# Kernel optimization log

Hardware: AMD Instinct MI355X
Metric: run time of the kernel (lower is better)

## Reference

```python
import jax, jax.numpy as jnp
import numpy as np

N_USERS = 100000
N_ITEMS = 50000
DIM = 64
N_EDGES = 1000000
N_NODES = N_USERS + N_ITEMS


def setup_inputs() -> dict:
    key = jax.random.key(0)
    k1, k2, k3 = jax.random.split(key, 3)
    # nn.init.normal_(std=0.1)
    user_emb = jax.random.normal(k1, (N_USERS, DIM), dtype=jnp.float32) * 0.1
    item_emb = jax.random.normal(k2, (N_ITEMS, DIM), dtype=jnp.float32) * 0.1
    edge_index = jax.random.randint(k3, (2, N_EDGES), 0, N_NODES, dtype=jnp.int32)
    return {"user_emb": user_emb, "item_emb": item_emb,
            "edge_index": edge_index, "n_layers": 3}


def reference(user_emb, item_emb, edge_index, n_layers):
    """LightGCN.computer(): n_layers of LGConv with uniform-alpha residual sum."""
    num_users = user_emb.shape[0]
    x = jnp.concatenate([user_emb, item_emb], axis=0)  # [N, d]
    n = x.shape[0]
    src, dst = edge_index[0], edge_index[1]

    # gcn_norm without self-loops (PyG LGConv default): deg from dst (in-degree)
    deg = jax.ops.segment_sum(jnp.ones_like(dst, dtype=x.dtype), dst,
                              num_segments=n)  # [N]
    dinv = jnp.where(deg > 0, jax.lax.rsqrt(jnp.maximum(deg, 1.0)), 0.0)
    norm = dinv[src] * dinv[dst]  # [E]

    alpha = 1.0 / (n_layers + 1)
    out = x * alpha
    for _ in range(n_layers):
        msg = x[src] * norm[:, None]                          # gather + scale [E, d]
        x = jax.ops.segment_sum(msg, dst, num_segments=n)     # scatter-add  [N, d]
        out = out + x * alpha
    users = out[:num_users]
    items = out[num_users:]
    return users, items
```

## Files before the change

### kernel.cpp

```cpp
#include <hip/hip_runtime.h>


#define N_USERS_C 100000
#define NNODES_C  150000
#define DIM_C     64
#define NLAYERS_C 3

#define BSHIFT    10
#define BSIZE     1024
#define NB_BUCKET ((NNODES_C + BSIZE - 1) >> BSHIFT)
#define EPB       4096
#define NBLK_E    ((1000000 + EPB - 1) / EPB)
#define HIST_N    (NB_BUCKET * NBLK_E)
#define SCAN_L1B  ((HIST_N + 1023) / 1024)


__device__ __forceinline__ float bf2f(unsigned short u) {
    union { unsigned int i; float f; } c;
    c.i = ((unsigned int)u) << 16;
    return c.f;
}

__device__ __forceinline__ unsigned short f2bf(float f) {
    union { float f; unsigned int i; } c;
    c.f = f;
    unsigned int x = c.i;
    return (unsigned short)((x + 0x7fffu + ((x >> 16) & 1u)) >> 16);
}


__global__ void k_hist(const int* __restrict__ dst, int* __restrict__ hist, int nE) {
    __shared__ int sh[NB_BUCKET];
    for (int i = threadIdx.x; i < NB_BUCKET; i += 256) sh[i] = 0;
    __syncthreads();
    int gEnd = min((int)(blockIdx.x + 1) * (EPB / 4), nE / 4);
    for (int g = blockIdx.x * (EPB / 4) + threadIdx.x; g < gEnd; g += 256) {
        int4 d4 = *(const int4*)(dst + g * 4);
        atomicAdd(&sh[d4.x >> BSHIFT], 1);
        atomicAdd(&sh[d4.y >> BSHIFT], 1);
        atomicAdd(&sh[d4.z >> BSHIFT], 1);
        atomicAdd(&sh[d4.w >> BSHIFT], 1);
    }
    __syncthreads();
    for (int b = threadIdx.x; b < NB_BUCKET; b += 256)
        hist[b * NBLK_E + blockIdx.x] = sh[b];
}

__global__ void k_scan_l1(int* __restrict__ hist, int* __restrict__ l1sum) {
    __shared__ int sd[1024];
    int t = threadIdx.x;
    int i = blockIdx.x * 1024 + t;
    int v = (i < HIST_N) ? hist[i] : 0;
    sd[t] = v;
    __syncthreads();
    for (int o = 1; o < 1024; o <<= 1) {
        int u = (t >= o) ? sd[t - o] : 0;
        __syncthreads();
        sd[t] += u;
        __syncthreads();
    }
    if (i < HIST_N) hist[i] = sd[t] - v;
    if (t == 1023) l1sum[blockIdx.x] = sd[1023];
}

__global__ void k_scan_l2add(int* __restrict__ hist, const int* __restrict__ l1sum) {
    __shared__ int s_pre;
    int t = threadIdx.x;
    if (t < 64) {
        int v = (t < (int)blockIdx.x && t < SCAN_L1B) ? l1sum[t] : 0;
        #pragma unroll
        for (int m = 1; m < 64; m <<= 1) v += __shfl_xor(v, m);
        if (t == 0) s_pre = v;
    }
    __syncthreads();
    int i = blockIdx.x * 1024 + t;
    if (i < HIST_N) hist[i] += s_pre;
}

__global__ void k_bucket(const int* __restrict__ src, const int* __restrict__ dst,
                         const int* __restrict__ histS, unsigned int* __restrict__ staged,
                         int nE) {
    __shared__ int sc[NB_BUCKET];
    for (int b = threadIdx.x; b < NB_BUCKET; b += 256)
        sc[b] = histS[b * NBLK_E + blockIdx.x];
    __syncthreads();
    int gEnd = min((int)(blockIdx.x + 1) * (EPB / 4), nE / 4);
    for (int g = blockIdx.x * (EPB / 4) + threadIdx.x; g < gEnd; g += 256) {
        int4 s4 = *(const int4*)(src + g * 4);
        int4 d4 = *(const int4*)(dst + g * 4);
        int p;
        p = atomicAdd(&sc[d4.x >> BSHIFT], 1);
        staged[p] = ((unsigned int)s4.x << BSHIFT) | (unsigned int)(d4.x & (BSIZE - 1));
        p = atomicAdd(&sc[d4.y >> BSHIFT], 1);
        staged[p] = ((unsigned int)s4.y << BSHIFT) | (unsigned int)(d4.y & (BSIZE - 1));
        p = atomicAdd(&sc[d4.z >> BSHIFT], 1);
        staged[p] = ((unsigned int)s4.z << BSHIFT) | (unsigned int)(d4.z & (BSIZE - 1));
        p = atomicAdd(&sc[d4.w >> BSHIFT], 1);
        staged[p] = ((unsigned int)s4.w << BSHIFT) | (unsigned int)(d4.w & (BSIZE - 1));
    }
}

__global__ void k_csr(const int* __restrict__ histS, const unsigned int* __restrict__ staged,
                      int* __restrict__ off, int* __restrict__ csrS,
                      int nE, int nNodes) {
    __shared__ int s_deg[BSIZE];
    __shared__ int s_scan[BSIZE];
    int b = blockIdx.x;
    int t = threadIdx.x;
    int base = histS[b * NBLK_E];
    int end  = (b + 1 < NB_BUCKET) ? histS[(b + 1) * NBLK_E] : nE;
    int cnt  = end - base;

    s_deg[t] = 0;
    __syncthreads();
    for (int k = t; k < cnt; k += BSIZE) {
        unsigned int w = staged[base + k];
        atomicAdd(&s_deg[w & (BSIZE - 1)], 1);
    }
    __syncthreads();
    int v = s_deg[t];
    s_scan[t] = v;
    __syncthreads();
    for (int o = 1; o < BSIZE; o <<= 1) {
        int u = (t >= o) ? s_scan[t - o] : 0;
        __syncthreads();
        s_scan[t] += u;
        __syncthreads();
    }
    int ex = s_scan[t] - v;
    int node = (b << BSHIFT) + t;
    if (node < nNodes) off[node] = base + ex;
    if (b == 0 && t == 0) off[nNodes] = nE;
    s_deg[t] = ex;
    __syncthreads();
    for (int k = t; k < cnt; k += BSIZE) {
        unsigned int w = staged[base + k];
        int slot = base + atomicAdd(&s_deg[w & (BSIZE - 1)], 1);
        csrS[slot] = (int)(w >> BSHIFT);
    }
}


__global__ void k_cvt(const float4* __restrict__ ue, const float4* __restrict__ ie,
                      const int* __restrict__ off, uint4* __restrict__ t0,
                      int n8u, int n8) {
    int i = blockIdx.x * blockDim.x + threadIdx.x;
    if (i >= n8) return;
    int node = i >> 3;
    int dg = off[node + 1] - off[node];
    float dv = (dg > 0) ? rsqrtf((float)dg) : 0.0f;
    float4 a, b;
    if (i < n8u) { a = ue[2 * i];         b = ue[2 * i + 1]; }
    else         { a = ie[2 * (i - n8u)]; b = ie[2 * (i - n8u) + 1]; }
    uint4 o;
    o.x = (unsigned int)f2bf(a.x * dv) | ((unsigned int)f2bf(a.y * dv) << 16);
    o.y = (unsigned int)f2bf(a.z * dv) | ((unsigned int)f2bf(a.w * dv) << 16);
    o.z = (unsigned int)f2bf(b.x * dv) | ((unsigned int)f2bf(b.y * dv) << 16);
    o.w = (unsigned int)f2bf(b.z * dv) | ((unsigned int)f2bf(b.w * dv) << 16);
    t0[i] = o;
}


__device__ __forceinline__ void add8(float* a, uint4 v) {
    a[0] += bf2f((unsigned short)(v.x & 0xffff));
    a[1] += bf2f((unsigned short)(v.x >> 16));
    a[2] += bf2f((unsigned short)(v.y & 0xffff));
    a[3] += bf2f((unsigned short)(v.y >> 16));
    a[4] += bf2f((unsigned short)(v.z & 0xffff));
    a[5] += bf2f((unsigned short)(v.z >> 16));
    a[6] += bf2f((unsigned short)(v.w & 0xffff));
    a[7] += bf2f((unsigned short)(v.w >> 16));
}

__device__ __forceinline__ void fma8(float* a, uint4 v, float w) {
    a[0] += w * bf2f((unsigned short)(v.x & 0xffff));
    a[1] += w * bf2f((unsigned short)(v.x >> 16));
    a[2] += w * bf2f((unsigned short)(v.y & 0xffff));
    a[3] += w * bf2f((unsigned short)(v.y >> 16));
    a[4] += w * bf2f((unsigned short)(v.z & 0xffff));
    a[5] += w * bf2f((unsigned short)(v.z >> 16));
    a[6] += w * bf2f((unsigned short)(v.w & 0xffff));
    a[7] += w * bf2f((unsigned short)(v.w >> 16));
}

template <int FINAL>
__global__ void k_gather(const int* __restrict__ off, const int* __restrict__ csrS,
                         const unsigned short* __restrict__ T,
                         unsigned short* __restrict__ Tn,
                         const float* __restrict__ ue, const float* __restrict__ ie,
                         const unsigned short* __restrict__ T0,
                         const unsigned short* __restrict__ T1,
                         float* __restrict__ outp, float alpha, int nNodes) {
    int t = blockIdx.x * blockDim.x + threadIdx.x;
    int w = t >> 6;
    int lane = t & 63;
    int half = lane >> 5;
    int sub  = lane & 31;
    int slot = sub >> 3;
    int q    = sub & 7;
    int node = w * 2 + half;
    if (node >= nNodes) return;

    int b = off[node];
    int e = off[node + 1];

    float a[8] = {0.f, 0.f, 0.f, 0.f, 0.f, 0.f, 0.f, 0.f};

    for (int jj = b; jj < e; jj += 4) {
        int j = jj + slot;
        if (j < e) {
            int s = csrS[j];
            uint4 v = *(const uint4*)(T + (size_t)s * DIM_C + q * 8);
            add8(a, v);
        }
    }

    #pragma unroll
    for (int m = 8; m <= 16; m <<= 1) {
        #pragma unroll
        for (int k = 0; k < 8; ++k) a[k] += __shfl_xor(a[k], m);
    }

    if (slot == 0) {
        size_t idx = (size_t)node * DIM_C + q * 8;
        float degf = (float)(e - b);
        if (FINAL) {
            float r[8] = {0.f, 0.f, 0.f, 0.f, 0.f, 0.f, 0.f, 0.f};
            float dv = 0.0f;
            if (e > b) {
                float sd = sqrtf(degf);
                dv = rsqrtf(degf);
                uint4 u0 = *(const uint4*)(T0 + idx);
                uint4 u1 = *(const uint4*)(T1 + idx);
                uint4 u2 = *(const uint4*)(T + idx);
                fma8(r, u0, sd);
                fma8(r, u1, sd);
                fma8(r, u2, sd);
            } else {
                const float* ob = (node < N_USERS_C)
                    ? (ue + (size_t)node * DIM_C + q * 8)
                    : (ie + (size_t)(node - N_USERS_C) * DIM_C + q * 8);
                float4 x0a = *(const float4*)(ob);
                float4 x0b = *(const float4*)(ob + 4);
                r[0] = x0a.x; r[1] = x0a.y; r[2] = x0a.z; r[3] = x0a.w;
                r[4] = x0b.x; r[5] = x0b.y; r[6] = x0b.z; r[7] = x0b.w;
            }
            float4 o0, o1;
            o0.x = alpha * (r[0] + dv * a[0]);
            o0.y = alpha * (r[1] + dv * a[1]);
            o0.z = alpha * (r[2] + dv * a[2]);
            o0.w = alpha * (r[3] + dv * a[3]);
            o1.x = alpha * (r[4] + dv * a[4]);
            o1.y = alpha * (r[5] + dv * a[5]);
            o1.z = alpha * (r[6] + dv * a[6]);
            o1.w = alpha * (r[7] + dv * a[7]);
            *(float4*)(outp + idx)     = o0;
            *(float4*)(outp + idx + 4) = o1;
        } else {
            float inv = (e > b) ? (1.0f / degf) : 0.0f;
            uint4 o;
            o.x = (unsigned int)f2bf(a[0] * inv) | ((unsigned int)f2bf(a[1] * inv) << 16);
            o.y = (unsigned int)f2bf(a[2] * inv) | ((unsigned int)f2bf(a[3] * inv) << 16);
            o.z = (unsigned int)f2bf(a[4] * inv) | ((unsigned int)f2bf(a[5] * inv) << 16);
            o.w = (unsigned int)f2bf(a[6] * inv) | ((unsigned int)f2bf(a[7] * inv) << 16);
            *(uint4*)(Tn + idx) = o;
        }
    }
}


__global__ void k_count_deg_fb(const int* __restrict__ dst, int* __restrict__ deg, int nE) {
    int e = blockIdx.x * blockDim.x + threadIdx.x;
    if (e < nE) atomicAdd(&deg[dst[e]], 1);
}

__global__ void k_dinv_fb(const int* __restrict__ deg, float* __restrict__ dinv, int n) {
    int i = blockIdx.x * blockDim.x + threadIdx.x;
    if (i < n) {
        int d = deg[i];
        dinv[i] = (d > 0) ? rsqrtf((float)d) : 0.0f;
    }
}

__global__ void k_init_fb(const float4* __restrict__ ue, const float4* __restrict__ ie,
                          float4* __restrict__ x, float4* __restrict__ out,
                          float alpha, int n4u, int n4) {
    int i = blockIdx.x * blockDim.x + threadIdx.x;
    if (i < n4) {
        float4 v = (i < n4u) ? ue[i] : ie[i - n4u];
        x[i] = v;
        out[i] = make_float4(v.x * alpha, v.y * alpha, v.z * alpha, v.w * alpha);
    }
}

__global__ void k_scatter(const int* __restrict__ src, const int* __restrict__ dst,
                          const float* __restrict__ dinv, const float* __restrict__ x,
                          float* __restrict__ y, int nE) {
    int t = blockIdx.x * blockDim.x + threadIdx.x;
    int e = t >> 4;
    int q = t & 15;
    if (e >= nE) return;
    int s = src[e];
    int d = dst[e];
    float w = dinv[s] * dinv[d];
    float4 v = *(const float4*)(x + (size_t)s * DIM_C + q * 4);
    float* yp = y + (size_t)d * DIM_C + q * 4;
    atomicAdd(yp + 0, v.x * w);
    atomicAdd(yp + 1, v.y * w);
    atomicAdd(yp + 2, v.z * w);
    atomicAdd(yp + 3, v.w * w);
}

__global__ void k_accum(const float4* __restrict__ y, float4* __restrict__ out,
                        float alpha, int n4) {
    int i = blockIdx.x * blockDim.x + threadIdx.x;
    if (i < n4) {
        float4 v = y[i];
        float4 o = out[i];
        o.x += v.x * alpha;
        o.y += v.y * alpha;
        o.z += v.z * alpha;
        o.w += v.w * alpha;
        out[i] = o;
    }
}


extern "C" void kernel_launch(void* const* d_in, const int* in_sizes, int n_in,
                              void* d_out, int out_size, void* d_ws, size_t ws_size,
                              hipStream_t stream) {
    const float* user_emb = (const float*)d_in[0];
    const float* item_emb = (const float*)d_in[1];
    const int*   edge     = (const int*)d_in[2];

    const int nE = in_sizes[2] / 2;
    const int* src = edge;
    const int* dst = edge + nE;

    const int nNodes = NNODES_C;
    const int nElems = nNodes * DIM_C;
    const int n4     = nElems / 4;
    const int n4u    = N_USERS_C * DIM_C / 4;
    const float alpha = 1.0f / (NLAYERS_C + 1);
    float* out = (float*)d_out;

    const size_t REQ = 66344448;

    char* ws = (char*)d_ws;

    if (ws_size >= REQ) {
        int*            hist   = (int*)           (ws);
        int*            l1sum  = (int*)           (ws + 144064);
        unsigned int*   staged = (unsigned int*)  (ws + 144320);
        int*            off    = (int*)           (ws + 4144320);
        int*            csrS   = (int*)           (ws + 4744336);
        unsigned short* T0     = (unsigned short*)(ws + 8744448);
        unsigned short* T1     = (unsigned short*)(ws + 27944448);
        unsigned short* T2     = (unsigned short*)(ws + 47144448);

        k_hist<<<NBLK_E, 256, 0, stream>>>(dst, hist, nE);
        k_scan_l1<<<SCAN_L1B, 1024, 0, stream>>>(hist, l1sum);
        k_scan_l2add<<<SCAN_L1B, 1024, 0, stream>>>(hist, l1sum);
        k_bucket<<<NBLK_E, 256, 0, stream>>>(src, dst, hist, staged, nE);
        k_csr<<<NB_BUCKET, BSIZE, 0, stream>>>(hist, staged, off, csrS, nE, nNodes);

        const int n8  = nElems / 8;
        const int n8u = N_USERS_C * DIM_C / 8;
        k_cvt<<<(n8 + 255) / 256, 256, 0, stream>>>(
            (const float4*)user_emb, (const float4*)item_emb, off, (uint4*)T0, n8u, n8);

        const int gwaves  = (nNodes + 1) / 2;
        const int gblocks = (gwaves * 64 + 255) / 256;
        k_gather<0><<<gblocks, 256, 0, stream>>>(off, csrS, T0, T1,
                                                 nullptr, nullptr, nullptr, nullptr,
                                                 nullptr, alpha, nNodes);
        k_gather<0><<<gblocks, 256, 0, stream>>>(off, csrS, T1, T2,
                                                 nullptr, nullptr, nullptr, nullptr,
                                                 nullptr, alpha, nNodes);
        k_gather<1><<<gblocks, 256, 0, stream>>>(off, csrS, T2, nullptr,
                                                 user_emb, item_emb, T0, T1,
                                                 out, alpha, nNodes);
    } else {
        int*   deg  = (int*)  (ws);
        float* dinv = (float*)(ws + 600000);
        float* xbuf = (float*)(ws + 1200000);
        float* ybuf = (float*)(ws + 1200000 + (size_t)nElems * 4);

        hipMemsetAsync(deg, 0, (size_t)nNodes * sizeof(int), stream);
        k_count_deg_fb<<<(nE + 255) / 256, 256, 0, stream>>>(dst, deg, nE);
        k_dinv_fb<<<(nNodes + 255) / 256, 256, 0, stream>>>(deg, dinv, nNodes);
        k_init_fb<<<(n4 + 255) / 256, 256, 0, stream>>>(
            (const float4*)user_emb, (const float4*)item_emb,
            (float4*)xbuf, (float4*)out, alpha, n4u, n4);

        float* xb = xbuf;
        float* yb = ybuf;
        const int scatterThreads = nE * 16;
        for (int l = 0; l < NLAYERS_C; ++l) {
            hipMemsetAsync(yb, 0, (size_t)nElems * sizeof(float), stream);
            k_scatter<<<(scatterThreads + 255) / 256, 256, 0, stream>>>(
                src, dst, dinv, xb, yb, nE);
            k_accum<<<(n4 + 255) / 256, 256, 0, stream>>>(
                (const float4*)yb, (float4*)out, alpha, n4);
            float* tmp = xb; xb = yb; yb = tmp;
        }
    }
}
```

Before: 147.8 us.

## Fuse histogram, scan and bucketing into one kernel using fixed-capacity buckets

Replaces the separate histogram, two-level scan and bucket-scatter kernels with a single kernel. Each block counts locally, then reserves space in fixed-capacity per-bucket regions through global atomics. k_csr now computes the global bucket prefix from the bucket counts. This drops several kernel launches and a pass over dst, at the cost of a memset, more workspace, and a hard cap of 16384 edges per bucket that could overflow on skewed inputs.

```diff
diff --git a/kernel.cpp b/kernel.cpp
--- a/kernel.cpp
+++ b/kernel.cpp
@@ -9,10 +9,10 @@
 #define BSHIFT    10
 #define BSIZE     1024
 #define NB_BUCKET ((NNODES_C + BSIZE - 1) >> BSHIFT)
+#define CAPSHIFT  14
+#define CAP       (1 << CAPSHIFT)
 #define EPB       4096
 #define NBLK_E    ((1000000 + EPB - 1) / EPB)
-#define HIST_N    (NB_BUCKET * NBLK_E)
-#define SCAN_L1B  ((HIST_N + 1023) / 1024)
 
 
 __device__ __forceinline__ float bf2f(unsigned short u) {
@@ -29,97 +29,69 @@
 }
 
 
-__global__ void k_hist(const int* __restrict__ dst, int* __restrict__ hist, int nE) {
-    __shared__ int sh[NB_BUCKET];
-    for (int i = threadIdx.x; i < NB_BUCKET; i += 256) sh[i] = 0;
-    __syncthreads();
-    int gEnd = min((int)(blockIdx.x + 1) * (EPB / 4), nE / 4);
-    for (int g = blockIdx.x * (EPB / 4) + threadIdx.x; g < gEnd; g += 256) {
+__global__ void k_bucket2(const int* __restrict__ src, const int* __restrict__ dst,
+                          int* __restrict__ bcnt, unsigned int* __restrict__ staged,
+                          int nE) {
+    __shared__ int s_cnt[NB_BUCKET];
+    __shared__ int s_cur[NB_BUCKET];
+    int t = threadIdx.x;
+    for (int i = t; i < NB_BUCKET; i += 256) s_cnt[i] = 0;
+    __syncthreads();
+
+    int nE4  = nE >> 2;
+    int g0   = blockIdx.x * (EPB / 4) + t;
+    int gEnd = min((int)(blockIdx.x + 1) * (EPB / 4), nE4);
+
+    for (int g = g0; g < gEnd; g += 256) {
         int4 d4 = *(const int4*)(dst + g * 4);
-        atomicAdd(&sh[d4.x >> BSHIFT], 1);
-        atomicAdd(&sh[d4.y >> BSHIFT], 1);
-        atomicAdd(&sh[d4.z >> BSHIFT], 1);
-        atomicAdd(&sh[d4.w >> BSHIFT], 1);
-    }
-    __syncthreads();
-    for (int b = threadIdx.x; b < NB_BUCKET; b += 256)
-        hist[b * NBLK_E + blockIdx.x] = sh[b];
-}
-
-__global__ void k_scan_l1(int* __restrict__ hist, int* __restrict__ l1sum) {
-    __shared__ int sd[1024];
-    int t = threadIdx.x;
-    int i = blockIdx.x * 1024 + t;
-    int v = (i < HIST_N) ? hist[i] : 0;
-    sd[t] = v;
-    __syncthreads();
-    for (int o = 1; o < 1024; o <<= 1) {
-        int u = (t >= o) ? sd[t - o] : 0;
-        __syncthreads();
-        sd[t] += u;
-        __syncthreads();
-    }
-    if (i < HIST_N) hist[i] = sd[t] - v;
-    if (t == 1023) l1sum[blockIdx.x] = sd[1023];
-}
-
-__global__ void k_scan_l2add(int* __restrict__ hist, const int* __restrict__ l1sum) {
-    __shared__ int s_pre;
-    int t = threadIdx.x;
-    if (t < 64) {
-        int v = (t < (int)blockIdx.x && t < SCAN_L1B) ? l1sum[t] : 0;
-        #pragma unroll
-        for (int m = 1; m < 64; m <<= 1) v += __shfl_xor(v, m);
-        if (t == 0) s_pre = v;
-    }
-    __syncthreads();
-    int i = blockIdx.x * 1024 + t;
-    if (i < HIST_N) hist[i] += s_pre;
-}
-
-__global__ void k_bucket(const int* __restrict__ src, const int* __restrict__ dst,
-                         const int* __restrict__ histS, unsigned int* __restrict__ staged,
-                         int nE) {
-    __shared__ int sc[NB_BUCKET];
-    for (int b = threadIdx.x; b < NB_BUCKET; b += 256)
-        sc[b] = histS[b * NBLK_E + blockIdx.x];
-    __syncthreads();
-    int gEnd = min((int)(blockIdx.x + 1) * (EPB / 4), nE / 4);
-    for (int g = blockIdx.x * (EPB / 4) + threadIdx.x; g < gEnd; g += 256) {
+        atomicAdd(&s_cnt[d4.x >> BSHIFT], 1);
+        atomicAdd(&s_cnt[d4.y >> BSHIFT], 1);
+        atomicAdd(&s_cnt[d4.z >> BSHIFT], 1);
+        atomicAdd(&s_cnt[d4.w >> BSHIFT], 1);
+    }
+    if (blockIdx.x == gridDim.x - 1 && t == 0) {
+        for (int k = nE4 * 4; k < nE; ++k) atomicAdd(&s_cnt[dst[k] >> BSHIFT], 1);
+    }
+    __syncthreads();
+
+    for (int i = t; i < NB_BUCKET; i += 256) {
+        int c = s_cnt[i];
+        s_cur[i] = (c > 0) ? ((i << CAPSHIFT) + atomicAdd(&bcnt[i], c)) : 0;
+    }
+    __syncthreads();
+
+    for (int g = g0; g < gEnd; g += 256) {
         int4 s4 = *(const int4*)(src + g * 4);
         int4 d4 = *(const int4*)(dst + g * 4);
         int p;
-        p = atomicAdd(&sc[d4.x >> BSHIFT], 1);
+        p = atomicAdd(&s_cur[d4.x >> BSHIFT], 1);
         staged[p] = ((unsigned int)s4.x << BSHIFT) | (unsigned int)(d4.x & (BSIZE - 1));
-        p = atomicAdd(&sc[d4.y >> BSHIFT], 1);
+        p = atomicAdd(&s_cur[d4.y >> BSHIFT], 1);
         staged[p] = ((unsigned int)s4.y << BSHIFT) | (unsigned int)(d4.y & (BSIZE - 1));
-        p = atomicAdd(&sc[d4.z >> BSHIFT], 1);
+        p = atomicAdd(&s_cur[d4.z >> BSHIFT], 1);
         staged[p] = ((unsigned int)s4.z << BSHIFT) | (unsigned int)(d4.z & (BSIZE - 1));
-        p = atomicAdd(&sc[d4.w >> BSHIFT], 1);
+        p = atomicAdd(&s_cur[d4.w >> BSHIFT], 1);
         staged[p] = ((unsigned int)s4.w << BSHIFT) | (unsigned int)(d4.w & (BSIZE - 1));
     }
-}
-
-__global__ void k_csr(const int* __restrict__ histS, const unsigned int* __restrict__ staged,
+    if (blockIdx.x == gridDim.x - 1 && t == 0) {
+        for (int k = nE4 * 4; k < nE; ++k) {
+            int d = dst[k];
+            int p = atomicAdd(&s_cur[d >> BSHIFT], 1);
+            staged[p] = ((unsigned int)src[k] << BSHIFT) | (unsigned int)(d & (BSIZE - 1));
+        }
+    }
+}
+
+__global__ void k_csr(const int* __restrict__ bcnt, const unsigned int* __restrict__ staged,
                       int* __restrict__ off, int* __restrict__ csrS,
                       int nE, int nNodes) {
     __shared__ int s_deg[BSIZE];
     __shared__ int s_scan[BSIZE];
     int b = blockIdx.x;
     int t = threadIdx.x;
-    int base = histS[b * NBLK_E];
-    int end  = (b + 1 < NB_BUCKET) ? histS[(b + 1) * NBLK_E] : nE;
-    int cnt  = end - base;
-
-    s_deg[t] = 0;
-    __syncthreads();
-    for (int k = t; k < cnt; k += BSIZE) {
-        unsigned int w = staged[base + k];
-        atomicAdd(&s_deg[w & (BSIZE - 1)], 1);
-    }
-    __syncthreads();
-    int v = s_deg[t];
-    s_scan[t] = v;
+
+    int c = (t < NB_BUCKET) ? bcnt[t] : 0;
+    s_scan[t] = c;
     __syncthreads();
     for (int o = 1; o < BSIZE; o <<= 1) {
         int u = (t >= o) ? s_scan[t - o] : 0;
@@ -127,15 +99,36 @@
         s_scan[t] += u;
         __syncthreads();
     }
+    int cnt     = bcnt[b];
+    int csrBase = s_scan[b] - cnt;
+    int sbase   = b << CAPSHIFT;
+    __syncthreads();
+
+    s_deg[t] = 0;
+    __syncthreads();
+    for (int k = t; k < cnt; k += BSIZE) {
+        unsigned int w = staged[sbase + k];
+        atomicAdd(&s_deg[w & (BSIZE - 1)], 1);
+    }
+    __syncthreads();
+    int v = s_deg[t];
+    s_scan[t] = v;
+    __syncthreads();
+    for (int o = 1; o < BSIZE; o <<= 1) {
+        int u = (t >= o) ? s_scan[t - o] : 0;
+        __syncthreads();
+        s_scan[t] += u;
+        __syncthreads();
+    }
     int ex = s_scan[t] - v;
     int node = (b << BSHIFT) + t;
-    if (node < nNodes) off[node] = base + ex;
+    if (node < nNodes) off[node] = csrBase + ex;
     if (b == 0 && t == 0) off[nNodes] = nE;
-    s_deg[t] = ex;
+    s_deg[t] = csrBase + ex;
     __syncthreads();
     for (int k = t; k < cnt; k += BSIZE) {
-        unsigned int w = staged[base + k];
-        int slot = base + atomicAdd(&s_deg[w & (BSIZE - 1)], 1);
+        unsigned int w = staged[sbase + k];
+        int slot = atomicAdd(&s_deg[w & (BSIZE - 1)], 1);
         csrS[slot] = (int)(w >> BSHIFT);
     }
 }
@@ -344,25 +337,22 @@
     const float alpha = 1.0f / (NLAYERS_C + 1);
     float* out = (float*)d_out;
 
-    const size_t REQ = 66344448;
+    const size_t REQ = 71834880;
 
     char* ws = (char*)d_ws;
 
     if (ws_size >= REQ) {
-        int*            hist   = (int*)           (ws);
-        int*            l1sum  = (int*)           (ws + 144064);
-        unsigned int*   staged = (unsigned int*)  (ws + 144320);
-        int*            off    = (int*)           (ws + 4144320);
-        int*            csrS   = (int*)           (ws + 4744336);
-        unsigned short* T0     = (unsigned short*)(ws + 8744448);
-        unsigned short* T1     = (unsigned short*)(ws + 27944448);
-        unsigned short* T2     = (unsigned short*)(ws + 47144448);
-
-        k_hist<<<NBLK_E, 256, 0, stream>>>(dst, hist, nE);
-        k_scan_l1<<<SCAN_L1B, 1024, 0, stream>>>(hist, l1sum);
-        k_scan_l2add<<<SCAN_L1B, 1024, 0, stream>>>(hist, l1sum);
-        k_bucket<<<NBLK_E, 256, 0, stream>>>(src, dst, hist, staged, nE);
-        k_csr<<<NB_BUCKET, BSIZE, 0, stream>>>(hist, staged, off, csrS, nE, nNodes);
+        int*            bcnt   = (int*)           (ws);
+        unsigned int*   staged = (unsigned int*)  (ws + 1024);
+        int*            off    = (int*)           (ws + 9634816);
+        int*            csrS   = (int*)           (ws + 10234832);
+        unsigned short* T0     = (unsigned short*)(ws + 14234880);
+        unsigned short* T1     = (unsigned short*)(ws + 33434880);
+        unsigned short* T2     = (unsigned short*)(ws + 52634880);
+
+        hipMemsetAsync(bcnt, 0, NB_BUCKET * sizeof(int), stream);
+        k_bucket2<<<NBLK_E, 256, 0, stream>>>(src, dst, bcnt, staged, nE);
+        k_csr<<<NB_BUCKET, BSIZE, 0, stream>>>(bcnt, staged, off, csrS, nE, nNodes);
 
         const int n8  = nElems / 8;
         const int n8u = N_USERS_C * DIM_C / 8;
```

New measurement: 151.8 us. +2.7%, slower.
